# Optimization experiments

Hardware: AMD Instinct MI355X
Metric: run time of the kernel (lower is better)

The kernel has to match this reference:

```python
import jax, jax.numpy as jnp
import numpy as np

N, C, IN_DIM, H_DIM, NUM_DEP = 16384, 4, 300, 512, 48


def setup_inputs() -> dict:
    key = jax.random.key(0)
    ks = jax.random.split(key, 12)
    # --- tree structure: 4-ary heap, reversed so children have SMALLER index than parent; root = N-1 ---
    i = np.arange(N)
    j = (N - 1) - i                                   # heap index (root j=0)
    cj = C * j[:, None] + 1 + np.arange(C)[None, :]   # heap indices of children [N,C]
    valid = cj <= N - 1
    child_idx = np.where(valid, (N - 1) - cj, 0).astype(np.int32)
    mask_h = valid.astype(np.float32)
    mask_e = valid.astype(np.float32)
    rng = np.random.default_rng(0)
    child_dep = rng.integers(0, NUM_DEP, size=(N, C)).astype(np.int32)
    leaf = ~valid.any(axis=1)
    # torch leaf branch: one virtual child with h=zeros and dep index 0
    mask_e[leaf, 0] = 1.0
    child_dep[leaf, 0] = 0
    child_idx[leaf, 0] = 0
    s = 0.02  # weight scale (stands in for xavier init)
    lin = lambda k, o, d: (jax.random.normal(k, (o, d), jnp.float32) * s)
    return {
        "x": jax.random.normal(ks[0], (N, IN_DIM), jnp.float32),
        "child_idx": jnp.asarray(child_idx),
        "child_dep": jnp.asarray(child_dep),
        "mask_h": jnp.asarray(mask_h),
        "mask_e": jnp.asarray(mask_e),
        "demb": jax.random.normal(ks[1], (NUM_DEP, H_DIM), jnp.float32) * s,
        "iux_w": lin(ks[2], 2 * H_DIM, IN_DIM), "iux_b": jnp.zeros((2 * H_DIM,), jnp.float32),
        "iuh_w": lin(ks[3], 2 * H_DIM, H_DIM), "iuh_b": jnp.zeros((2 * H_DIM,), jnp.float32),
        "iue_w": lin(ks[4], 2 * H_DIM, H_DIM), "iue_b": jnp.zeros((2 * H_DIM,), jnp.float32),
        "fx_w": lin(ks[5], H_DIM, IN_DIM), "fx_b": jnp.zeros((H_DIM,), jnp.float32),
        "fh_w": lin(ks[6], H_DIM, H_DIM), "fh_b": jnp.zeros((H_DIM,), jnp.float32),
        "fe_w": lin(ks[7], H_DIM, H_DIM), "fe_b": jnp.zeros((H_DIM,), jnp.float32),
    }


def reference(x, child_idx, child_dep, mask_h, mask_e, demb,
              iux_w, iux_b, iuh_w, iuh_b, iue_w, iue_b,
              fx_w, fx_b, fh_w, fh_b, fe_w, fe_b):
    n, h_dim = x.shape[0], fh_w.shape[0]

    def step(H, xs):
        t, xt, cidx, cdep, mh, me = xs
        ch = H[cidx] * mh[:, None]            # [C,h] child hiddens (zeros for pad / leaf virtual child)
        e = demb[cdep]                        # [C,h] dependency embeddings
        h_sum = ch.sum(0)                     # child-sum h
        e_sum = (e * me[:, None]).sum(0)      # child-sum dep embedding (leaf -> demb[0])
        iu = (xt @ iux_w.T + iux_b) + (h_sum @ iuh_w.T + iuh_b) + (e_sum @ iue_w.T + iue_b)
        i_g = jax.nn.sigmoid(iu[:h_dim])
        u = jnp.tanh(iu[h_dim:])
        f = jax.nn.sigmoid(ch @ fh_w.T + fh_b + (xt @ fx_w.T + fx_b) + e @ fe_w.T + fe_b)  # [C,h]
        h_new = jnp.tanh(i_g * u + (f * ch).sum(0))   # padded rows contribute 0 since ch=0
        return H.at[t].set(h_new), None

    H0 = jnp.zeros((n, h_dim), x.dtype)
    xs = (jnp.arange(n), x, child_idx, child_dep, mask_h, mask_e)
    Hf, _ = jax.lax.scan(step, H0, xs)
    return Hf[n - 1][None, :]   # root hidden state, shape [1, h_dim]
```

## Files before the change

kernel.cpp:

```cpp
#include <hip/hip_runtime.h>
#include <cstddef>

#define N_NODES 16384
#define HD      512
#define INDIM   300
#define INP     320
#define NDEP    48
#define NLEAF   10923
#define NINT    5461
#define KT      32
#define LM      16
#define LCOL    128

typedef unsigned int u32;
typedef unsigned short u16;
typedef __attribute__((ext_vector_type(8))) short short8;
typedef __attribute__((ext_vector_type(4))) float f32x4;

typedef __attribute__((address_space(1))) const u32 as1_u32;
typedef __attribute__((address_space(3))) u32 as3_u32;

__device__ __forceinline__ float sigmoidf_(float v) {
    return 1.f / (1.f + __expf(-v));
}
__device__ __forceinline__ float tanhf_(float v) {
    v = fminf(15.f, fmaxf(-15.f, v));
    const float e = __expf(2.f * v);
    return (e - 1.f) / (e + 1.f);
}
__device__ __forceinline__ u16 f2bf(float f) {
    u32 u = __float_as_uint(f);
    u32 r = (u + 0x7fffu + ((u >> 16) & 1u)) >> 16;
    return (u16)r;
}
__device__ __forceinline__ float b2f(u16 v) {
    return __uint_as_float((u32)v << 16);
}
__device__ __forceinline__ u32 pack2(float a, float b) {
    return (u32)f2bf(a) | ((u32)f2bf(b) << 16);
}

#define RA  (N_NODES * 75)
#define RB  (N_NODES * 10)
#define RC1 (1536 * 75)
#define RC2 (1536 * 10)
#define RD  (1536 * 128)
#define CV_TOT (RA + RB + RC1 + RC2 + RD)

__global__ __launch_bounds__(256)
void convert_vec_kernel(const float* __restrict__ x,
                        const float* __restrict__ iux_w, const float* __restrict__ fx_w,
                        const float* __restrict__ iuh_w, const float* __restrict__ fh_w,
                        u16* __restrict__ xb, u16* __restrict__ WXb, u16* __restrict__ WHb)
{
    int idx = blockIdx.x * 256 + threadIdx.x;
    if (idx < RA) {
        const int r = idx / 75, k4 = idx - r * 75;
        const float4 v = *reinterpret_cast<const float4*>(x + (size_t)r * INDIM + k4 * 4);
        *reinterpret_cast<uint2*>(&xb[(size_t)r * INP + k4 * 4]) =
            make_uint2(pack2(v.x, v.y), pack2(v.z, v.w));
        return;
    }
    idx -= RA;
    if (idx < RB) {
        const int r = idx / 10, j = idx - r * 10;
        reinterpret_cast<u32*>(xb)[(size_t)r * 160 + 150 + j] = 0u;
        return;
    }
    idx -= RB;
    if (idx < RC1) {
        const int r = idx / 75, k4 = idx - r * 75;
        const float* src = (r < 1024) ? (iux_w + (size_t)r * INDIM)
                                      : (fx_w + (size_t)(r - 1024) * INDIM);
        const float4 v = *reinterpret_cast<const float4*>(src + k4 * 4);
        *reinterpret_cast<uint2*>(&WXb[(size_t)r * INP + k4 * 4]) =
            make_uint2(pack2(v.x, v.y), pack2(v.z, v.w));
        return;
    }
    idx -= RC1;
    if (idx < RC2) {
        const int r = idx / 10, j = idx - r * 10;
        reinterpret_cast<u32*>(WXb)[(size_t)r * 160 + 150 + j] = 0u;
        return;
    }
    idx -= RC2;
    {
        const int r = idx >> 7, k4 = idx & 127;
        const float* src = (r < 1024) ? (iuh_w + (size_t)r * HD)
                                      : (fh_w + (size_t)(r - 1024) * HD);
        const float4 v = *reinterpret_cast<const float4*>(src + k4 * 4);
        *reinterpret_cast<uint2*>(&WHb[(size_t)r * HD + k4 * 4]) =
            make_uint2(pack2(v.x, v.y), pack2(v.z, v.w));
    }
}

__device__ __forceinline__
void gemm_body(u16* As, u16* Bs,
               const u16* __restrict__ A, int lda,
               const u16* __restrict__ B, int ldb,
               u16* __restrict__ C, int ldc,
               int M, int K, int bx, int by)
{
    const int tid  = threadIdx.x;
    const int lane = tid & 63;
    const int wave = tid >> 6;
    const int mBlk = bx * 128;
    const int nBlk = by * 128;

    const int wr = (wave >> 1) * 64;
    const int wc = (wave & 1) * 64;
    const int fr = lane & 15;
    const int kg = lane >> 4;

    f32x4 acc[4][4];
    #pragma unroll
    for (int i = 0; i < 4; ++i)
        #pragma unroll
        for (int j = 0; j < 4; ++j) acc[i][j] = (f32x4){0.f, 0.f, 0.f, 0.f};

    int offA[4], offB[4];
    #pragma unroll
    for (int it = 0; it < 4; ++it) {
        const int s   = it * 256 + tid;
        const int row = s >> 3, c = s & 7;
        const int cs  = c ^ (row & 7);
        int ga = mBlk + row; if (ga > M - 1) ga = M - 1;
        offA[it] = ga * lda + cs * 8;
        offB[it] = (nBlk + row) * ldb + cs * 8;
    }

    for (int k0 = 0; k0 < K; k0 += 64) {
        #pragma unroll
        for (int it = 0; it < 4; ++it) {
            const int ldsOff = (it * 256 + wave * 64) * 8;
            __builtin_amdgcn_global_load_lds((as1_u32*)(A + offA[it] + k0),
                                             (as3_u32*)(&As[ldsOff]), 16, 0, 0);
            __builtin_amdgcn_global_load_lds((as1_u32*)(B + offB[it] + k0),
                                             (as3_u32*)(&Bs[ldsOff]), 16, 0, 0);
        }
        __syncthreads();
        #pragma unroll
        for (int half = 0; half < 2; ++half) {
            const int ckb = half * 4 + kg;
            short8 af[4], bf[4];
            #pragma unroll
            for (int f = 0; f < 4; ++f) {
                const int ar = wr + f * 16 + fr;
                af[f] = *(const short8*)&As[ar * 64 + ((ckb ^ (ar & 7)) * 8)];
                const int br = wc + f * 16 + fr;
                bf[f] = *(const short8*)&Bs[br * 64 + ((ckb ^ (br & 7)) * 8)];
            }
            #pragma unroll
            for (int mi = 0; mi < 4; ++mi)
                #pragma unroll
                for (int ni = 0; ni < 4; ++ni)
                    acc[mi][ni] = __builtin_amdgcn_mfma_f32_16x16x32_bf16(
                                      af[mi], bf[ni], acc[mi][ni], 0, 0, 0);
        }
        __syncthreads();
    }

    #pragma unroll
    for (int mi = 0; mi < 4; ++mi) {
        const int r0 = mBlk + wr + mi * 16 + kg * 4;
        #pragma unroll
        for (int v = 0; v < 4; ++v) {
            const int r = r0 + v;
            if (r >= M) continue;
            u16* crow = C + (size_t)r * ldc + nBlk + wc + fr;
            #pragma unroll
            for (int ni = 0; ni < 4; ++ni)
                crow[ni * 16] = f2bf(acc[mi][ni][v]);
        }
    }
}

__global__ __launch_bounds__(256, 4)
void xp_gemm_emb_kernel(const u16* __restrict__ xb, const u16* __restrict__ WXb,
                        u16* __restrict__ XPiub, u16* __restrict__ XPfb,
                        int gx1, int n1, int gx2, int nG,
                        const float* __restrict__ demb,
                        const float* __restrict__ iue_w, const float* __restrict__ fe_w,
                        const float* __restrict__ iux_b, const float* __restrict__ iuh_b,
                        const float* __restrict__ iue_b, const float* __restrict__ fx_b,
                        const float* __restrict__ fh_b, const float* __restrict__ fe_b,
                        float* __restrict__ iemb, float* __restrict__ femb,
                        float* __restrict__ ibc, float* __restrict__ fbc)
{
    __shared__ u16 As[128 * 64];
    __shared__ u16 Bs[128 * 64];
    const int flat = blockIdx.x;
    if (flat < nG) {
        if (flat < n1) {
            gemm_body(As, Bs, xb, INP, WXb, INP, XPiub, 1024, N_NODES, INP,
                      flat % gx1, flat / gx1);
        } else {
            const int f2 = flat - n1;
            gemm_body(As, Bs, xb + (size_t)NLEAF * INP, INP,
                      WXb + (size_t)1024 * INP, INP, XPfb, 512, NINT, INP,
                      f2 % gx2, f2 / gx2);
        }
        return;
    }
    const int bo  = flat - nG;
    const int tid = threadIdx.x;
    if (bo == 384) {
        for (int o = tid; o < 1024; o += 256) ibc[o] = iux_b[o] + iuh_b[o] + iue_b[o];
        for (int o = tid; o < 512;  o += 256) fbc[o] = fx_b[o] + fh_b[o] + fe_b[o];
        return;
    }
    const int wave = tid >> 6;
    const int d    = tid & 63;
    const bool isI = (bo < 256);
    const int o    = (isI ? bo : bo - 256) * 4 + wave;
    if (d >= NDEP) return;
    const float* wrow = isI ? (iue_w + (size_t)o * HD) : (fe_w + (size_t)o * HD);
    const float* drow = demb + (size_t)d * HD;

    float4 a0 = make_float4(0.f, 0.f, 0.f, 0.f);
    float4 a1 = make_float4(0.f, 0.f, 0.f, 0.f);
    for (int k = 0; k < HD; k += 8) {
        const float4 wv0 = *reinterpret_cast<const float4*>(wrow + k);
        const float4 wv1 = *reinterpret_cast<const float4*>(wrow + k + 4);
        const float4 dv0 = *reinterpret_cast<const float4*>(drow + k);
        const float4 dv1 = *reinterpret_cast<const float4*>(drow + k + 4);
        a0.x = fmaf(dv0.x, wv0.x, a0.x); a0.y = fmaf(dv0.y, wv0.y, a0.y);
        a0.z = fmaf(dv0.z, wv0.z, a0.z); a0.w = fmaf(dv0.w, wv0.w, a0.w);
        a1.x = fmaf(dv1.x, wv1.x, a1.x); a1.y = fmaf(dv1.y, wv1.y, a1.y);
        a1.z = fmaf(dv1.z, wv1.z, a1.z); a1.w = fmaf(dv1.w, wv1.w, a1.w);
    }
    const float s = ((a0.x + a0.y) + (a0.z + a0.w)) + ((a1.x + a1.y) + (a1.z + a1.w));
    if (isI) iemb[(size_t)d * 1024 + o] = s;
    else     femb[(size_t)d * 512  + o] = s;
}

__global__ __launch_bounds__(256, 4)
void gemm_bf16_dual_kernel(const u16* __restrict__ A1, int lda1,
                           const u16* __restrict__ B1, int ldb1,
                           u16* __restrict__ C1, int ldc1, int M1, int K1,
                           int gx1, int n1,
                           const u16* __restrict__ A2, int lda2,
                           const u16* __restrict__ B2, int ldb2,
                           u16* __restrict__ C2, int ldc2, int M2, int K2,
                           int gx2)
{
    __shared__ u16 As[128 * 64];
    __shared__ u16 Bs[128 * 64];
    const int flat = blockIdx.x;
    if (flat < n1) {
        gemm_body(As, Bs, A1, lda1, B1, ldb1, C1, ldc1, M1, K1,
                  flat % gx1, flat / gx1);
    } else {
        const int f2 = flat - n1;
        gemm_body(As, Bs, A2, lda2, B2, ldb2, C2, ldc2, M2, K2,
                  f2 % gx2, f2 / gx2);
    }
}

__global__ __launch_bounds__(256)
void fused_leaf_kernel(const u16* __restrict__ XPiub,
                       const float* __restrict__ iemb, const float* __restrict__ ibc,
                       const int* __restrict__ cidx, const float* __restrict__ mh,
                       u16* __restrict__ Hb, u16* __restrict__ HSB, int loNext)
{
    const int g   = blockIdx.x;
    const int p   = loNext + g;
    const int j2  = threadIdx.x * 2;

    int ct[4]; float cm[4];
    #pragma unroll
    for (int c = 0; c < 4; ++c) { ct[c] = cidx[p * 4 + c]; cm[c] = mh[p * 4 + c]; }

    const float2 ibci = *reinterpret_cast<const float2*>(&ibc[j2]);
    const float2 ibcu = *reinterpret_cast<const float2*>(&ibc[512 + j2]);
    const float2 iei  = *reinterpret_cast<const float2*>(&iemb[j2]);
    const float2 ieu  = *reinterpret_cast<const float2*>(&iemb[512 + j2]);

    float hs0 = 0.f, hs1 = 0.f;
    #pragma unroll
    for (int c = 0; c < 4; ++c) {
        if (cm[c] == 0.f) continue;
        const int t = ct[c];
        const u32 xi = *reinterpret_cast<const u32*>(&XPiub[(size_t)t * 1024 + j2]);
        const u32 xu = *reinterpret_cast<const u32*>(&XPiub[(size_t)t * 1024 + 512 + j2]);
        const float h0 = tanhf_(sigmoidf_(b2f((u16)xi) + iei.x + ibci.x)
                                * tanhf_(b2f((u16)xu) + ieu.x + ibcu.x));
        const float h1 = tanhf_(sigmoidf_(b2f((u16)(xi >> 16)) + iei.y + ibci.y)
                                * tanhf_(b2f((u16)(xu >> 16)) + ieu.y + ibcu.y));
        *reinterpret_cast<u32*>(&Hb[(size_t)t * 512 + j2]) = pack2(h0, h1);
        hs0 += h0; hs1 += h1;
    }
    *reinterpret_cast<u32*>(&HSB[(size_t)g * 512 + j2]) = pack2(hs0, hs1);
}

__global__ __launch_bounds__(256)
void fused_combine_kernel(const u16* __restrict__ XPiub, const u16* __restrict__ XPfb,
                          const u16* __restrict__ PIUb, const u16* __restrict__ GFb,
                          const int* __restrict__ cidx, const int* __restrict__ cdep,
                          const float* __restrict__ mh, const float* __restrict__ me,
                          const float* __restrict__ iemb, const float* __restrict__ femb,
                          const float* __restrict__ ibc, const float* __restrict__ fbc,
                          u16* __restrict__ Hb, u16* __restrict__ HSB,
                          int lo, int loNext, int isRoot, float* __restrict__ outp)
{
    const int j2 = threadIdx.x * 2;

    int ct[4]; float cm[4];
    if (isRoot) {
        ct[0] = N_NODES - 1; cm[0] = 1.f;
        ct[1] = ct[2] = ct[3] = 0; cm[1] = cm[2] = cm[3] = 0.f;
    } else {
        const int p = loNext + blockIdx.x;
        #pragma unroll
        for (int c = 0; c < 4; ++c) { ct[c] = cidx[p * 4 + c]; cm[c] = mh[p * 4 + c]; }
    }

    const float2 ibci = *reinterpret_cast<const float2*>(&ibc[j2]);
    const float2 ibcu = *reinterpret_cast<const float2*>(&ibc[512 + j2]);
    const float2 fbc2 = *reinterpret_cast<const float2*>(&fbc[j2]);

    float hs0 = 0.f, hs1 = 0.f;
    #pragma unroll
    for (int c = 0; c < 4; ++c) {
        if (cm[c] == 0.f) continue;
        const int t = ct[c];

        int ci2[4], dp2[4]; float m2[4], e2[4];
        #pragma unroll
        for (int k = 0; k < 4; ++k) {
            ci2[k] = cidx[t * 4 + k]; dp2[k] = cdep[t * 4 + k];
            m2[k]  = mh[t * 4 + k];   e2[k]  = me[t * 4 + k];
        }

        float ei0 = 0.f, ei1 = 0.f, eu0 = 0.f, eu1 = 0.f;
        #pragma unroll
        for (int k = 0; k < 4; ++k) {
            if (e2[k] != 0.f) {
                const float* ie = iemb + (size_t)dp2[k] * 1024;
                const float2 a = *reinterpret_cast<const float2*>(&ie[j2]);
                const float2 b = *reinterpret_cast<const float2*>(&ie[512 + j2]);
                ei0 = fmaf(e2[k], a.x, ei0); ei1 = fmaf(e2[k], a.y, ei1);
                eu0 = fmaf(e2[k], b.x, eu0); eu1 = fmaf(e2[k], b.y, eu1);
            }
        }

        const u32 xi = *reinterpret_cast<const u32*>(&XPiub[(size_t)t * 1024 + j2]);
        const u32 xu = *reinterpret_cast<const u32*>(&XPiub[(size_t)t * 1024 + 512 + j2]);
        const u32 pi = *reinterpret_cast<const u32*>(&PIUb[(size_t)(t - lo) * 1024 + j2]);
        const u32 pu = *reinterpret_cast<const u32*>(&PIUb[(size_t)(t - lo) * 1024 + 512 + j2]);
        const u32 xf = *reinterpret_cast<const u32*>(&XPfb[(size_t)(t - NLEAF) * 512 + j2]);

        const float iu_i0 = b2f((u16)xi) + b2f((u16)pi) + ibci.x + ei0;
        const float iu_i1 = b2f((u16)(xi >> 16)) + b2f((u16)(pi >> 16)) + ibci.y + ei1;
        const float iu_u0 = b2f((u16)xu) + b2f((u16)pu) + ibcu.x + eu0;
        const float iu_u1 = b2f((u16)(xu >> 16)) + b2f((u16)(pu >> 16)) + ibcu.y + eu1;
        const float xf0 = b2f((u16)xf) + fbc2.x;
        const float xf1 = b2f((u16)(xf >> 16)) + fbc2.y;

        float fcs0 = 0.f, fcs1 = 0.f;
        #pragma unroll
        for (int k = 0; k < 4; ++k) {
            if (m2[k] != 0.f) {
                const u32 gf = *reinterpret_cast<const u32*>(&GFb[(size_t)ci2[k] * 512 + j2]);
                const u32 hb = *reinterpret_cast<const u32*>(&Hb[(size_t)ci2[k] * 512 + j2]);
                const float2 fe = *reinterpret_cast<const float2*>(&femb[(size_t)dp2[k] * 512 + j2]);
                const float fv0 = b2f((u16)gf) + xf0 + fe.x;
                const float fv1 = b2f((u16)(gf >> 16)) + xf1 + fe.y;
                fcs0 = fmaf(sigmoidf_(fv0), m2[k] * b2f((u16)hb), fcs0);
                fcs1 = fmaf(sigmoidf_(fv1), m2[k] * b2f((u16)(hb >> 16)), fcs1);
            }
        }

        const float h0 = tanhf_(fmaf(sigmoidf_(iu_i0), tanhf_(iu_u0), fcs0));
        const float h1 = tanhf_(fmaf(sigmoidf_(iu_i1), tanhf_(iu_u1), fcs1));
        *reinterpret_cast<u32*>(&Hb[(size_t)t * 512 + j2]) = pack2(h0, h1);
        hs0 += h0; hs1 += h1;
        if (isRoot) *reinterpret_cast<float2*>(&outp[j2]) = make_float2(h0, h1);
    }
    if (!isRoot)
        *reinterpret_cast<u32*>(&HSB[(size_t)blockIdx.x * 512 + j2]) = pack2(hs0, hs1);
}

__global__ __launch_bounds__(256)
void emb_setup_kernel(const float* __restrict__ demb,
                      const float* __restrict__ iue_w,
                      const float* __restrict__ fe_w,
                      const float* __restrict__ iux_b,
                      const float* __restrict__ iuh_b,
                      const float* __restrict__ iue_b,
                      const float* __restrict__ fx_b,
                      const float* __restrict__ fh_b,
                      const float* __restrict__ fe_b,
                      float* __restrict__ iemb,
                      float* __restrict__ femb,
                      float* __restrict__ ibc,
                      float* __restrict__ fbc)
{
    const int d   = blockIdx.x;
    const int tid = threadIdx.x;
    __shared__ float sd[HD];
    sd[tid]       = demb[d * HD + tid];
    sd[tid + 256] = demb[d * HD + 256 + tid];
    __syncthreads();

    #pragma unroll
    for (int r = 0; r < 4; ++r) {
        const int o = r * 256 + tid;
        const float* w = iue_w + (size_t)o * HD;
        float acc = 0.f;
        for (int k = 0; k < HD; k += 4) {
            const float4 wv = *reinterpret_cast<const float4*>(w + k);
            acc += sd[k] * wv.x + sd[k + 1] * wv.y + sd[k + 2] * wv.z + sd[k + 3] * wv.w;
        }
        iemb[(size_t)d * 1024 + o] = acc;
    }
    #pragma unroll
    for (int r = 0; r < 2; ++r) {
        const int o = r * 256 + tid;
        const float* w = fe_w + (size_t)o * HD;
        float acc = 0.f;
        for (int k = 0; k < HD; k += 4) {
            const float4 wv = *reinterpret_cast<const float4*>(w + k);
            acc += sd[k] * wv.x + sd[k + 1] * wv.y + sd[k + 2] * wv.z + sd[k + 3] * wv.w;
        }
        femb[(size_t)d * HD + o] = acc;
    }
    if (d == 0) {
        #pragma unroll
        for (int r = 0; r < 4; ++r) { const int o = r * 256 + tid; ibc[o] = iux_b[o] + iuh_b[o] + iue_b[o]; }
        #pragma unroll
        for (int r = 0; r < 2; ++r) { const int o = r * 256 + tid; fbc[o] = fx_b[o] + fh_b[o] + fe_b[o]; }
    }
}

__global__ __launch_bounds__(256, 2)
void level_kernel(const float* __restrict__ x,
                  const int*   __restrict__ child_idx,
                  const int*   __restrict__ child_dep,
                  const float* __restrict__ mask_h,
                  const float* __restrict__ mask_e,
                  const float* __restrict__ iux_w,
                  const float* __restrict__ iuh_w,
                  const float* __restrict__ fx_w,
                  const float* __restrict__ fh_w,
                  const float* __restrict__ iemb,
                  const float* __restrict__ femb,
                  const float* __restrict__ ibc,
                  const float* __restrict__ fbc,
                  float* __restrict__ H,
                  int tLo, int tEnd)
{
    __shared__ __align__(16) float sA[KT][68];
    __shared__ float sWI[KT][LCOL + 1];
    __shared__ float sWU[KT][LCOL + 1];
    __shared__ float sWF[KT][LCOL + 1];
    __shared__ int   sCidx[LM][4];
    __shared__ float sMh[LM][4];
    __shared__ int   sDep[LM][4];
    __shared__ float sMe[LM][4];

    const int tid  = threadIdx.x;
    const int base = tLo + blockIdx.x * LM;
    const int j0   = blockIdx.y * LCOL;

    if (tid < LM * 4) {
        const int m = tid >> 2, c = tid & 3;
        const int t = base + m;
        const bool v = (t < tEnd);
        sCidx[m][c] = v ? child_idx[t * 4 + c] : 0;
        sMh[m][c]   = v ? mask_h[t * 4 + c]    : 0.f;
        sDep[m][c]  = v ? child_dep[t * 4 + c] : 0;
        sMe[m][c]   = v ? mask_e[t * 4 + c]    : 0.f;
    }

    const int jj = tid & 63;
    const int mg = tid >> 6;

    float acc_i[4][2], acc_u[4][2], acc_fx[4][2], acc_f[4][2][4];
    #pragma unroll
    for (int mm = 0; mm < 4; ++mm)
        #pragma unroll
        for (int c2 = 0; c2 < 2; ++c2) {
            acc_i[mm][c2] = 0.f; acc_u[mm][c2] = 0.f; acc_fx[mm][c2] = 0.f;
            #pragma unroll
            for (int c = 0; c < 4; ++c) acc_f[mm][c2][c] = 0.f;
        }

    __syncthreads();

    for (int k0 = 0; k0 < HD; k0 += KT) {
        #pragma unroll
        for (int it = 0; it < 2; ++it) {
            const int chunk = tid + it * 256;
            const int mc = chunk >> 3;
            const int kk = (chunk & 7) * 4;
            const int m = mc >> 2, c = mc & 3;
            const float mhv = sMh[m][c];
            float4 v = make_float4(0.f, 0.f, 0.f, 0.f);
            if (mhv != 0.f)
                v = *reinterpret_cast<const float4*>(H + (size_t)sCidx[m][c] * HD + k0 + kk);
            sA[kk + 0][mc] = v.x; sA[kk + 1][mc] = v.y; sA[kk + 2][mc] = v.z; sA[kk + 3][mc] = v.w;
        }
        #pragma unroll
        for (int it = 0; it < 4; ++it) {
            const int chunk = tid + it * 256;
            const int row = chunk >> 3;
            const int kk = (chunk & 7) * 4;
            const float4 vI = *reinterpret_cast<const float4*>(iuh_w + (size_t)(j0 + row) * HD + k0 + kk);
            const float4 vU = *reinterpret_cast<const float4*>(iuh_w + (size_t)(j0 + row + 512) * HD + k0 + kk);
            const float4 vF = *reinterpret_cast<const float4*>(fh_w  + (size_t)(j0 + row) * HD + k0 + kk);
            sWI[kk + 0][row] = vI.x; sWI[kk + 1][row] = vI.y; sWI[kk + 2][row] = vI.z; sWI[kk + 3][row] = vI.w;
            sWU[kk + 0][row] = vU.x; sWU[kk + 1][row] = vU.y; sWU[kk + 2][row] = vU.z; sWU[kk + 3][row] = vU.w;
            sWF[kk + 0][row] = vF.x; sWF[kk + 1][row] = vF.y; sWF[kk + 2][row] = vF.z; sWF[kk + 3][row] = vF.w;
        }
        __syncthreads();
        #pragma unroll 4
        for (int k = 0; k < KT; ++k) {
            const float wi0 = sWI[k][jj], wi1 = sWI[k][jj + 64];
            const float wu0 = sWU[k][jj], wu1 = sWU[k][jj + 64];
            const float wf0 = sWF[k][jj], wf1 = sWF[k][jj + 64];
            #pragma unroll
            for (int mm = 0; mm < 4; ++mm) {
                const int m = mg + mm * 4;
                const float4 cv = *reinterpret_cast<const float4*>(&sA[k][m * 4]);
                const float hs = (cv.x + cv.y) + (cv.z + cv.w);
                acc_i[mm][0] = fmaf(hs, wi0, acc_i[mm][0]);
                acc_i[mm][1] = fmaf(hs, wi1, acc_i[mm][1]);
                acc_u[mm][0] = fmaf(hs, wu0, acc_u[mm][0]);
                acc_u[mm][1] = fmaf(hs, wu1, acc_u[mm][1]);
                acc_f[mm][0][0] = fmaf(cv.x, wf0, acc_f[mm][0][0]);
                acc_f[mm][1][0] = fmaf(cv.x, wf1, acc_f[mm][1][0]);
                acc_f[mm][0][1] = fmaf(cv.y, wf0, acc_f[mm][0][1]);
                acc_f[mm][1][1] = fmaf(cv.y, wf1, acc_f[mm][1][1]);
                acc_f[mm][0][2] = fmaf(cv.z, wf0, acc_f[mm][0][2]);
                acc_f[mm][1][2] = fmaf(cv.z, wf1, acc_f[mm][1][2]);
                acc_f[mm][0][3] = fmaf(cv.w, wf0, acc_f[mm][0][3]);
                acc_f[mm][1][3] = fmaf(cv.w, wf1, acc_f[mm][1][3]);
            }
        }
        __syncthreads();
    }

    for (int k0 = 0; k0 < INDIM; k0 += KT) {
        if (tid < 128) {
            const int m = tid >> 3;
            const int kk = (tid & 7) * 4;
            const int t = base + m;
            float4 v = make_float4(0.f, 0.f, 0.f, 0.f);
            if (t < tEnd && (k0 + kk + 3) < INDIM)
                v = *reinterpret_cast<const float4*>(x + (size_t)t * INDIM + k0 + kk);
            sA[kk + 0][m] = v.x; sA[kk + 1][m] = v.y; sA[kk + 2][m] = v.z; sA[kk + 3][m] = v.w;
        }
        #pragma unroll
        for (int it = 0; it < 4; ++it) {
            const int chunk = tid + it * 256;
            const int row = chunk >> 3;
            const int kk = (chunk & 7) * 4;
            float4 vI = make_float4(0.f, 0.f, 0.f, 0.f), vU = vI, vF = vI;
            if ((k0 + kk + 3) < INDIM) {
                vI = *reinterpret_cast<const float4*>(iux_w + (size_t)(j0 + row) * INDIM + k0 + kk);
                vU = *reinterpret_cast<const float4*>(iux_w + (size_t)(j0 + row + 512) * INDIM + k0 + kk);
                vF = *reinterpret_cast<const float4*>(fx_w  + (size_t)(j0 + row) * INDIM + k0 + kk);
            }
            sWI[kk + 0][row] = vI.x; sWI[kk + 1][row] = vI.y; sWI[kk + 2][row] = vI.z; sWI[kk + 3][row] = vI.w;
            sWU[kk + 0][row] = vU.x; sWU[kk + 1][row] = vU.y; sWU[kk + 2][row] = vU.z; sWU[kk + 3][row] = vU.w;
            sWF[kk + 0][row] = vF.x; sWF[kk + 1][row] = vF.y; sWF[kk + 2][row] = vF.z; sWF[kk + 3][row] = vF.w;
        }
        __syncthreads();
        #pragma unroll 4
        for (int k = 0; k < KT; ++k) {
            const float wi0 = sWI[k][jj], wi1 = sWI[k][jj + 64];
            const float wu0 = sWU[k][jj], wu1 = sWU[k][jj + 64];
            const float wf0 = sWF[k][jj], wf1 = sWF[k][jj + 64];
            #pragma unroll
            for (int mm = 0; mm < 4; ++mm) {
                const float xv = sA[k][mg + mm * 4];
                acc_i[mm][0]  = fmaf(xv, wi0, acc_i[mm][0]);
                acc_i[mm][1]  = fmaf(xv, wi1, acc_i[mm][1]);
                acc_u[mm][0]  = fmaf(xv, wu0, acc_u[mm][0]);
                acc_u[mm][1]  = fmaf(xv, wu1, acc_u[mm][1]);
                acc_fx[mm][0] = fmaf(xv, wf0, acc_fx[mm][0]);
                acc_fx[mm][1] = fmaf(xv, wf1, acc_fx[mm][1]);
            }
        }
        __syncthreads();
    }

    #pragma unroll
    for (int mm = 0; mm < 4; ++mm) {
        const int m = mg + mm * 4;
        const int t = base + m;
        if (t >= tEnd) continue;
        #pragma unroll
        for (int c2 = 0; c2 < 2; ++c2) {
            const int j = j0 + c2 * 64 + jj;
            float emb_i = 0.f, emb_u = 0.f;
            #pragma unroll
            for (int c = 0; c < 4; ++c) {
                const float mev = sMe[m][c];
                if (mev != 0.f) {
                    const float* ie = iemb + (size_t)sDep[m][c] * 1024;
                    emb_i = fmaf(mev, ie[j], emb_i);
                    emb_u = fmaf(mev, ie[j + 512], emb_u);
                }
            }
            const float iu_i = acc_i[mm][c2] + ibc[j] + emb_i;
            const float iu_u = acc_u[mm][c2] + ibc[j + 512] + emb_u;
            const float ig = sigmoidf_(iu_i);
            const float uu = tanhf_(iu_u);
            float fcs = 0.f;
            #pragma unroll
            for (int c = 0; c < 4; ++c) {
                const float mhv = sMh[m][c];
                if (mhv != 0.f) {
                    const float fv = acc_f[mm][c2][c] + acc_fx[mm][c2] + fbc[j]
                                   + femb[(size_t)sDep[m][c] * HD + j];
                    const float fg = sigmoidf_(fv);
                    const float chj = H[(size_t)sCidx[m][c] * HD + j] * mhv;
                    fcs = fmaf(fg, chj, fcs);
                }
            }
            H[(size_t)t * HD + j] = tanhf_(fmaf(ig, uu, fcs));
        }
    }
}

__global__ void copy_out_kernel(const float* __restrict__ H, float* __restrict__ out) {
    const int j = blockIdx.x * 256 + threadIdx.x;
    if (j < HD) out[j] = H[(size_t)(N_NODES - 1) * HD + j];
}

static const int lvlLo[9] = {0, 10923, 15019, 16043, 16299, 16363, 16379, 16383, 16384};
static const int lvlN[8]  = {10923, 4096, 1024, 256, 64, 16, 4, 1};

extern "C" void kernel_launch(void* const* d_in, const int* in_sizes, int n_in,
                              void* d_out, int out_size, void* d_ws, size_t ws_size,
                              hipStream_t stream)
{
    const float* x     = (const float*)d_in[0];
    const int*   cidx  = (const int*)  d_in[1];
    const int*   cdep  = (const int*)  d_in[2];
    const float* mh    = (const float*)d_in[3];
    const float* me    = (const float*)d_in[4];
    const float* demb  = (const float*)d_in[5];
    const float* iux_w = (const float*)d_in[6];
    const float* iux_b = (const float*)d_in[7];
    const float* iuh_w = (const float*)d_in[8];
    const float* iuh_b = (const float*)d_in[9];
    const float* iue_w = (const float*)d_in[10];
    const float* iue_b = (const float*)d_in[11];
    const float* fx_w  = (const float*)d_in[12];
    const float* fx_b  = (const float*)d_in[13];
    const float* fh_w  = (const float*)d_in[14];
    const float* fh_b  = (const float*)d_in[15];
    const float* fe_w  = (const float*)d_in[16];
    const float* fe_b  = (const float*)d_in[17];

    const size_t szHb  = (size_t)N_NODES * HD * 2;
    const size_t szXPi = (size_t)N_NODES * 1024 * 2;
    const size_t szXPf = (size_t)NINT * 512 * 2;
    const size_t szGF  = (size_t)N_NODES * HD * 2;
    const size_t szPIU = (size_t)4096 * 1024 * 2;
    const size_t szHSB = (size_t)4096 * 512 * 2;
    const size_t szXB  = (size_t)N_NODES * INP * 2;
    const size_t szWX  = (size_t)1536 * INP * 2;
    const size_t szWH  = (size_t)1536 * HD * 2;
    const size_t szIE  = (size_t)NDEP * 1024 * 4;
    const size_t szFE  = (size_t)NDEP * 512 * 4;
    const size_t szIB  = 4096, szFB = 2048;
    const size_t need = szHb + szXPi + szXPf + szGF + szPIU + szHSB
                      + szXB + szWX + szWH + szIE + szFE + szIB + szFB;

    if (ws_size >= need) {
        char* w = (char*)d_ws;
        u16*   Hb    = (u16*)w;    w += szHb;
        u16*   XPiub = (u16*)w;    w += szXPi;
        u16*   XPfb  = (u16*)w;    w += szXPf;
        u16*   GFb   = (u16*)w;    w += szGF;
        u16*   PIUa  = (u16*)w;    w += szPIU;
        u16*   HSB   = (u16*)w;    w += szHSB;
        u16*   xb    = (u16*)w;    w += szXB;
        u16*   WXb   = (u16*)w;    w += szWX;
        u16*   WHb   = (u16*)w;    w += szWH;
        float* iemb  = (float*)w;  w += szIE;
        float* femb  = (float*)w;  w += szFE;
        float* ibc   = (float*)w;  w += szIB;
        float* fbc   = (float*)w;  w += szFB;

        hipLaunchKernelGGL(convert_vec_kernel, dim3(CV_TOT / 256), dim3(256), 0, stream,
                           x, iux_w, fx_w, iuh_w, fh_w, xb, WXb, WHb);

        {
            const int gx1 = N_NODES / 128, n1 = gx1 * (1024 / 128);
            const int gx2 = (NINT + 127) / 128;
            const int nG  = n1 + gx2 * (512 / 128);
            hipLaunchKernelGGL(xp_gemm_emb_kernel, dim3(nG + 385), dim3(256), 0, stream,
                               xb, WXb, XPiub, XPfb, gx1, n1, gx2, nG,
                               demb, iue_w, fe_w, iux_b, iuh_b, iue_b,
                               fx_b, fh_b, fe_b, iemb, femb, ibc, fbc);
        }

        hipLaunchKernelGGL(fused_leaf_kernel, dim3(lvlN[1]), dim3(256), 0, stream,
                           XPiub, iemb, ibc, cidx, mh, Hb, HSB, lvlLo[1]);

        for (int l = 1; l < 8; ++l) {
            const int pLo = lvlLo[l - 1], pN = lvlN[l - 1];
            const int lo  = lvlLo[l],     n  = lvlN[l];
            const int gx1 = (pN + 127) / 128, n1 = gx1 * (512 / 128);
            const int gx2 = (n + 127) / 128,  n2 = gx2 * (1024 / 128);
            hipLaunchKernelGGL(gemm_bf16_dual_kernel, dim3(n1 + n2), dim3(256), 0, stream,
                               Hb + (size_t)pLo * HD, HD, WHb + (size_t)1024 * HD, HD,
                               GFb + (size_t)pLo * HD, HD, pN, HD, gx1, n1,
                               HSB, HD, WHb, HD, PIUa, 1024, n, HD, gx2);
            const int isRoot = (l == 7);
            const int gridC  = isRoot ? 1 : lvlN[l + 1];
            const int loNext = isRoot ? 0 : lvlLo[l + 1];
            hipLaunchKernelGGL(fused_combine_kernel, dim3(gridC), dim3(256), 0, stream,
                               XPiub, XPfb, PIUa, GFb, cidx, cdep, mh, me,
                               iemb, femb, ibc, fbc, Hb, HSB,
                               lo, loNext, isRoot, (float*)d_out);
        }
        return;
    }

    float* ws   = (float*)d_ws;
    float* H    = ws;
    float* iembF = H + (size_t)N_NODES * HD;
    float* fembF = iembF + (size_t)NDEP * 1024;
    float* ibcF  = fembF + (size_t)NDEP * HD;
    float* fbcF  = ibcF + 1024;

    hipLaunchKernelGGL(emb_setup_kernel, dim3(NDEP), dim3(256), 0, stream,
                       demb, iue_w, fe_w, iux_b, iuh_b, iue_b, fx_b, fh_b, fe_b,
                       iembF, fembF, ibcF, fbcF);
    for (int l = 0; l < 8; ++l) {
        dim3 grid((lvlN[l] + LM - 1) / LM, HD / LCOL);
        hipLaunchKernelGGL(level_kernel, grid, dim3(256), 0, stream,
                           x, cidx, cdep, mh, me, iux_w, iuh_w, fx_w, fh_w,
                           iembF, fembF, ibcF, fbcF, H, lvlLo[l], lvlLo[l] + lvlN[l]);
    }
    hipLaunchKernelGGL(copy_out_kernel, dim3(2), dim3(256), 0, stream, H, (float*)d_out);
}
```

Baseline: 246.0 us.

## Double-buffer LDS tiles in bf16 GEMM body and reorder embedding blocks first

Adds a two-stage LDS ping-pong to the shared GEMM body: the next K tile is prefetched via global_load_lds while MFMAs consume the current one, which is meant to hide global load latency behind compute. LDS per block doubles and launch bounds drop from 4 to 2 blocks per CU, so occupancy falls. The fused xp/embedding kernel also now schedules the small embedding and bias blocks at the lowest block indices, ahead of the GEMM tiles. There is only one barrier per iteration, and the prefetch into the other buffer is issued before the MFMAs, so correctness relies on that barrier and on how the async LDS loads are waited on.

```diff
diff --git a/kernel.cpp b/kernel.cpp
--- a/kernel.cpp
+++ b/kernel.cpp
@@ -11,6 +11,7 @@
 #define KT      32
 #define LM      16
 #define LCOL    128
+#define TILE_E  8192
 
 typedef unsigned int u32;
 typedef unsigned short u16;
@@ -129,16 +130,31 @@
         offB[it] = (nBlk + row) * ldb + cs * 8;
     }
 
+    #pragma unroll
+    for (int it = 0; it < 4; ++it) {
+        const int ldsOff = (it * 256 + wave * 64) * 8;
+        __builtin_amdgcn_global_load_lds((as1_u32*)(A + offA[it]),
+                                         (as3_u32*)(&As[ldsOff]), 16, 0, 0);
+        __builtin_amdgcn_global_load_lds((as1_u32*)(B + offB[it]),
+                                         (as3_u32*)(&Bs[ldsOff]), 16, 0, 0);
+    }
+    __syncthreads();
+
+    int cur = 0;
     for (int k0 = 0; k0 < K; k0 += 64) {
-        #pragma unroll
-        for (int it = 0; it < 4; ++it) {
-            const int ldsOff = (it * 256 + wave * 64) * 8;
-            __builtin_amdgcn_global_load_lds((as1_u32*)(A + offA[it] + k0),
-                                             (as3_u32*)(&As[ldsOff]), 16, 0, 0);
-            __builtin_amdgcn_global_load_lds((as1_u32*)(B + offB[it] + k0),
-                                             (as3_u32*)(&Bs[ldsOff]), 16, 0, 0);
-        }
-        __syncthreads();
+        const int nxt = cur ^ 1;
+        if (k0 + 64 < K) {
+            #pragma unroll
+            for (int it = 0; it < 4; ++it) {
+                const int ldsOff = nxt * TILE_E + (it * 256 + wave * 64) * 8;
+                __builtin_amdgcn_global_load_lds((as1_u32*)(A + offA[it] + k0 + 64),
+                                                 (as3_u32*)(&As[ldsOff]), 16, 0, 0);
+                __builtin_amdgcn_global_load_lds((as1_u32*)(B + offB[it] + k0 + 64),
+                                                 (as3_u32*)(&Bs[ldsOff]), 16, 0, 0);
+            }
+        }
+        const u16* Ac = As + cur * TILE_E;
+        const u16* Bc = Bs + cur * TILE_E;
         #pragma unroll
         for (int half = 0; half < 2; ++half) {
             const int ckb = half * 4 + kg;
@@ -146,9 +162,9 @@
             #pragma unroll
             for (int f = 0; f < 4; ++f) {
                 const int ar = wr + f * 16 + fr;
-                af[f] = *(const short8*)&As[ar * 64 + ((ckb ^ (ar & 7)) * 8)];
+                af[f] = *(const short8*)&Ac[ar * 64 + ((ckb ^ (ar & 7)) * 8)];
                 const int br = wc + f * 16 + fr;
-                bf[f] = *(const short8*)&Bs[br * 64 + ((ckb ^ (br & 7)) * 8)];
+                bf[f] = *(const short8*)&Bc[br * 64 + ((ckb ^ (br & 7)) * 8)];
             }
             #pragma unroll
             for (int mi = 0; mi < 4; ++mi)
@@ -158,6 +174,7 @@
                                       af[mi], bf[ni], acc[mi][ni], 0, 0, 0);
         }
         __syncthreads();
+        cur = nxt;
     }
 
     #pragma unroll
@@ -175,7 +192,7 @@
     }
 }
 
-__global__ __launch_bounds__(256, 4)
+__global__ __launch_bounds__(256, 2)
 void xp_gemm_emb_kernel(const u16* __restrict__ xb, const u16* __restrict__ WXb,
                         u16* __restrict__ XPiub, u16* __restrict__ XPfb,
                         int gx1, int n1, int gx2, int nG,
@@ -187,22 +204,23 @@
                         float* __restrict__ iemb, float* __restrict__ femb,
                         float* __restrict__ ibc, float* __restrict__ fbc)
 {
-    __shared__ u16 As[128 * 64];
-    __shared__ u16 Bs[128 * 64];
+    __shared__ u16 As[2 * TILE_E];
+    __shared__ u16 Bs[2 * TILE_E];
     const int flat = blockIdx.x;
-    if (flat < nG) {
-        if (flat < n1) {
+    if (flat >= 385) {
+        const int g = flat - 385;
+        if (g < n1) {
             gemm_body(As, Bs, xb, INP, WXb, INP, XPiub, 1024, N_NODES, INP,
-                      flat % gx1, flat / gx1);
+                      g % gx1, g / gx1);
         } else {
-            const int f2 = flat - n1;
+            const int f2 = g - n1;
             gemm_body(As, Bs, xb + (size_t)NLEAF * INP, INP,
                       WXb + (size_t)1024 * INP, INP, XPfb, 512, NINT, INP,
                       f2 % gx2, f2 / gx2);
         }
         return;
     }
-    const int bo  = flat - nG;
+    const int bo  = flat;
     const int tid = threadIdx.x;
     if (bo == 384) {
         for (int o = tid; o < 1024; o += 256) ibc[o] = iux_b[o] + iuh_b[o] + iue_b[o];
@@ -234,7 +252,7 @@
     else     femb[(size_t)d * 512  + o] = s;
 }
 
-__global__ __launch_bounds__(256, 4)
+__global__ __launch_bounds__(256, 2)
 void gemm_bf16_dual_kernel(const u16* __restrict__ A1, int lda1,
                            const u16* __restrict__ B1, int ldb1,
                            u16* __restrict__ C1, int ldc1, int M1, int K1,
@@ -244,8 +262,8 @@
                            u16* __restrict__ C2, int ldc2, int M2, int K2,
                            int gx2)
 {
-    __shared__ u16 As[128 * 64];
-    __shared__ u16 Bs[128 * 64];
+    __shared__ u16 As[2 * TILE_E];
+    __shared__ u16 Bs[2 * TILE_E];
     const int flat = blockIdx.x;
     if (flat < n1) {
         gemm_body(As, Bs, A1, lda1, B1, ldb1, C1, ldc1, M1, K1,
```

After: 239.2 us. 2.8% less time.
